# Kernel tuning notes

Measured on AMD Instinct MI355X. Metric: run time of the kernel, lower is better.

## Reference

```python
import jax, jax.numpy as jnp
import numpy as np
from math import pi
from jax.scipy.linalg import expm

N_QUBITS = 9
DIM = 256
BATCH = 64
HID = (4 + DIM) // 2
D = 2 ** N_QUBITS
INTERACTION_WEIGHT = 866.0 / (3.0 ** 6)


def setup_inputs() -> dict:
    key = jax.random.key(0)
    k = jax.random.split(key, 6)
    x = jax.random.normal(k[0], (BATCH, DIM), dtype=jnp.float32)
    mask_batch = jax.random.uniform(k[1], (BATCH, N_QUBITS), dtype=jnp.float32)
    upper = (jax.random.uniform(k[2], (N_QUBITS, N_QUBITS)) < 0.4).astype(jnp.float32)
    upper = jnp.triu(upper, 1)
    adj = upper + upper.T  # symmetric 0/1, zero diagonal
    W1 = jax.random.normal(k[3], (DIM, HID), dtype=jnp.float32) / np.sqrt(DIM).astype(np.float32)
    b1 = jnp.zeros((HID,), jnp.float32)
    W2 = jax.random.normal(k[4], (HID, 4), dtype=jnp.float32) / np.sqrt(HID).astype(np.float32)
    b2 = jnp.zeros((4,), jnp.float32)
    return {"x": x, "mask_batch": mask_batch, "adj": adj, "W1": W1, "b1": b1, "W2": W2, "b2": b2}


def _forward(x, mask_batch, adj, W1, b1, W2, b2):
    c64 = jnp.complex64
    n = N_QUBITS
    b = x.shape[0]
    # varyer MLP -> [raw_omega, delta, raw_phi, raw_time]
    v = jax.nn.relu(x @ W1 + b1) @ W2 + b2
    omega = jax.nn.softplus(v[:, 0])
    delta = v[:, 1]
    phi = jnp.mod(v[:, 2], 2.0 * pi)
    t = jax.nn.softplus(v[:, 3])
    sx = jnp.array([[0, 1], [1, 0]], dtype=c64)
    sy = jnp.array([[0, -1j], [1j, 0]], dtype=c64)
    nop = jnp.array([[1, 0], [0, 0]], dtype=c64)  # (I + sigma_z)/2
    # single-qubit Hamiltonian, (b, 2, 2)
    h = ((omega / 2)[:, None, None].astype(c64)
         * (jnp.cos(phi)[:, None, None] * sx - jnp.sin(phi)[:, None, None] * sy)
         - delta[:, None, None].astype(c64) * nop)
    # H_single = sum_j mask[b,j] * (I_{2^j} (x) h[b] (x) I_{2^{n-1-j}})
    H = jnp.zeros((b, D, D), dtype=c64)
    for j in range(n):  # structural loop over qubits (n fixed, small)
        L, R = 2 ** j, 2 ** (n - 1 - j)
        Ej = jnp.einsum('pq,bxy,rs->bpxrqys',
                        jnp.eye(L, dtype=c64), h, jnp.eye(R, dtype=c64)).reshape(b, D, D)
        H = H + mask_batch[:, j, None, None].astype(c64) * Ej
    # Interaction term: n_i n_j operators are diagonal in the computational basis.
    # kron ordering puts qubit 0 most significant; n_op = diag(1, 0) -> occ = 1 - bit.
    s = jnp.arange(D)
    bit = (s[:, None] >> (n - 1 - jnp.arange(n))[None, :]) & 1  # (D, n)
    occ = (1 - bit).astype(jnp.float32)
    Wmat = INTERACTION_WEIGHT * adj[None] * mask_batch[:, :, None] * mask_batch[:, None, :]  # (b,n,n)
    diag = jnp.einsum('bij,si,sj->bs', Wmat, occ, occ)  # (b, D)
    idx = jnp.arange(D)
    H = H.at[:, idx, idx].add(diag.astype(c64))
    # time evolution: psi = expm(-i t H) |0...0>  (first column of the propagator)
    M = (-1j) * t[:, None, None].astype(c64) * H
    exp_h = jax.vmap(expm)(M)
    return exp_h[:, :, 0]


def reference(x, mask_batch, adj, W1, b1, W2, b2):
    return _forward(x, mask_batch, adj, W1, b1, W2, b2)
```

## Files before the change

### kernel.cpp

```cpp
#include <hip/hip_runtime.h>
#include <math.h>

#define NQ     9
#define NDIM   256
#define NHID   130
#define NST    512
#define NBATCH 64
#define MCAP   460

__device__ __forceinline__ float softplusf(float x) {
    return (x > 0.f) ? (x + log1pf(expf(-x))) : log1pf(expf(x));
}

template<int CTRL>
__device__ __forceinline__ float dpp_f(float v) {
    int i = __float_as_int(v);
    return __int_as_float(__builtin_amdgcn_update_dpp(i, i, CTRL, 0xF, 0xF, false));
}
__device__ __forceinline__ float swzx16(float v) {
    return __int_as_float(__builtin_amdgcn_ds_swizzle(__float_as_int(v), 0x401F));
}
__device__ __forceinline__ float bperm(int addr, float v) {
    return __int_as_float(__builtin_amdgcn_ds_bpermute(addr, __float_as_int(v)));
}

typedef unsigned uint2v __attribute__((ext_vector_type(2)));

__device__ __forceinline__ float lx16(float v, bool hi) {
#if __has_builtin(__builtin_amdgcn_permlane16_swap)
    uint2v r = __builtin_amdgcn_permlane16_swap(__float_as_uint(v), __float_as_uint(v), false, false);
    return __uint_as_float(hi ? r[0] : r[1]);
#else
    return swzx16(v);
#endif
}
__device__ __forceinline__ float lx32(float v, bool hi, int bpaddr) {
#if __has_builtin(__builtin_amdgcn_permlane32_swap)
    uint2v r = __builtin_amdgcn_permlane32_swap(__float_as_uint(v), __float_as_uint(v), false, false);
    return __uint_as_float(hi ? r[0] : r[1]);
#else
    return bperm(bpaddr, v);
#endif
}

#define MV(NR, CR)                                                            \
  do {                                                                        \
    _Pragma("unroll")                                                         \
    for (int r = 0; r < 8; ++r) {                                             \
      const float a = CR[r];                                                  \
      float yr = dg2[r] * a;                                                  \
      yr = fmaf(in2[0], CR[r^1], yr);                                         \
      yr = fmaf(in2[1], CR[r^2], yr);                                         \
      yr = fmaf(in2[2], CR[r^4], yr);                                         \
      yr = fmaf(cx2[0], dpp_f<0xB1>(a), yr);                                  \
      yr = fmaf(cx2[1], dpp_f<0x4E>(a), yr);                                  \
      const float a7 = dpp_f<0x141>(a);                                       \
      yr = fmaf(cx2[2], dpp_f<0x1B>(a7), yr);                                 \
      yr = fmaf(cx2[3], dpp_f<0x140>(a7), yr);                                \
      yr = fmaf(cx2[4], lx16(a, h16), yr);                                    \
      yr = fmaf(cx2[5], lx32(a, h32, bpaddr), yr);                            \
      NR[r] = yr - NR[r];                                                     \
    }                                                                         \
  } while (0)

#define COEF(P, K)                                                            \
  do { const float ck = 2.0f * jlf[K];                                        \
    switch ((K) & 3) {                                                        \
      case 0: _Pragma("unroll") for (int r=0;r<8;++r) accr[r] += ck*P[r]; break; \
      case 1: _Pragma("unroll") for (int r=0;r<8;++r) acci[r] -= ck*P[r]; break; \
      case 2: _Pragma("unroll") for (int r=0;r<8;++r) accr[r] -= ck*P[r]; break; \
      case 3: _Pragma("unroll") for (int r=0;r<8;++r) acci[r] += ck*P[r]; break; \
    }                                                                         \
  } while (0)

__global__ __launch_bounds__(256) void fused_kernel(
    const float* __restrict__ x,    const float* __restrict__ mask,
    const float* __restrict__ adj,  const float* __restrict__ W1,
    const float* __restrict__ b1,   const float* __restrict__ W2,
    const float* __restrict__ b2,   float* __restrict__ out)
{
    const int b    = blockIdx.x;
    const int tid  = threadIdx.x;
    const int w    = tid >> 6;
    const int lane = tid & 63;

    __shared__ __align__(16) float w1s[NDIM * NHID];
    __shared__ float xs[NDIM];
    __shared__ float hs[NHID + 2];
    __shared__ float vs[4];
    __shared__ float ms[NQ];
    __shared__ float Wm[81];
    __shared__ double Ssh;

    float Dsum[8], mo[8];

    if (w != 0) {
        const int t0 = tid - 64;
        const float4* W14 = (const float4*)W1;
        float4* d4 = (float4*)w1s;
        for (int i = t0; i < (NDIM*NHID)/4; i += 192) d4[i] = W14[i];
        if (t0 < NDIM/4) ((float4*)xs)[t0] = ((const float4*)(x + b*NDIM))[t0];
    } else {
        if (lane < NQ) ms[lane] = mask[b*NQ + lane];
        for (int e = lane; e < 81; e += 64) {
            int i = e / 9, j = e % 9;
            Wm[e] = (866.0f/729.0f) * adj[e] * ms[i] * ms[j];
        }
        #pragma unroll
        for (int r = 0; r < 8; ++r) {
            const int s = (lane << 3) | r;
            float d = 0.f, m = 0.f;
            #pragma unroll
            for (int i = 0; i < NQ; ++i) {
                float oi = ((s >> (8 - i)) & 1) ? 0.f : 1.f;
                m = fmaf(ms[i], oi, m);
                float row = 0.f;
                #pragma unroll
                for (int j = 0; j < NQ; ++j) {
                    float oj = ((s >> (8 - j)) & 1) ? 0.f : 1.f;
                    row = fmaf(Wm[i*9 + j], oj, row);
                }
                d = fmaf(oi, row, d);
            }
            Dsum[r] = d; mo[r] = m;
        }
    }
    __syncthreads();

    if (tid < NHID) {
        float a0 = b1[tid], a1 = 0.f;
        #pragma unroll 8
        for (int i = 0; i < NDIM; i += 2) {
            a0 = fmaf(xs[i],     w1s[i*NHID + tid],       a0);
            a1 = fmaf(xs[i + 1], w1s[(i + 1)*NHID + tid], a1);
        }
        hs[tid] = fmaxf(a0 + a1, 0.f);
    }
    __syncthreads();

    {
        float p = hs[lane]      * W2[lane*4 + w]
                + hs[lane + 64] * W2[(lane + 64)*4 + w];
        if (lane < 2) p += hs[128 + lane] * W2[(128 + lane)*4 + w];
        #pragma unroll
        for (int off = 32; off; off >>= 1) p += __shfl_down(p, off);
        if (lane == 0) vs[w] = p + b2[w];
    }
    __syncthreads();

    if (w != 0) return;

    double* fd  = (double*)w1s;
    float*  jlf = w1s + 2*(MCAP + 8);

    const float omega = softplusf(vs[0]);
    const float delta = vs[1];
    const float phi   = vs[2];
    const float t     = softplusf(vs[3]);
    const float halfw = 0.5f * omega;

    float Dd[8];
    #pragma unroll
    for (int r = 0; r < 8; ++r) Dd[r] = Dsum[r] - delta * mo[r];

    float mx = Dd[0], mn = Dd[0];
    #pragma unroll
    for (int r = 1; r < 8; ++r) { mx = fmaxf(mx, Dd[r]); mn = fminf(mn, Dd[r]); }
    #pragma unroll
    for (int off = 1; off < 64; off <<= 1) {
        mx = fmaxf(mx, __shfl_xor(mx, off));
        mn = fminf(mn, __shfl_xor(mn, off));
    }
    float sm = 0.f;
    #pragma unroll
    for (int j = 0; j < NQ; ++j) sm += ms[j];
    const float c0   = 0.5f * (mx + mn);
    const float rho  = (0.5f * (mx - mn) + halfw * sm) * 1.003f;
    const float rhoE = fmaxf(rho, 1e-20f);
    const float zc   = t * rho;

    int M;
    const bool tiny = (zc < 0.5f);
    if (tiny) M = 8;
    else {
        M = (int)ceilf(zc + 3.5f * cbrtf(zc + 4.f) + 4.f);
        if (M > MCAP) M = MCAP;
    }

    if (tiny) {
        if (lane <= 8) {
            const float zh = 0.5f * zc;
            const float q  = zh * zh;
            float fact = 1.f;
            for (int i = 2; i <= lane; ++i) fact *= (float)i;
            const float pw = (lane == 0) ? 1.f : powf(zh, (float)lane);
            jlf[lane] = (pw / fact) *
                (1.f - q/(float)(lane+1) + 0.5f*q*q/(float)((lane+1)*(lane+2)));
        }
    } else {
        if (lane == 0) {
            const double zz  = (double)zc;
            const double inv = 1.0 / zz;
            const int   M2   = M + 20 + M/10;
            double fkp1 = 0.0, fk = 1e-30;
            for (int k = M2; k >= 1; --k) {
                double fkm1 = 2.0 * (double)k * inv * fk - fkp1;
                fkp1 = fk; fk = fkm1;
                const int idx = k - 1;
                if (idx <= M) fd[idx] = fk;
            }
            double S = fd[0];
            for (int idx = 2; idx <= M; idx += 2) S += 2.0 * fd[idx];
            Ssh = S;
        }
        for (int k = lane; k <= M; k += 64) jlf[k] = (float)(fd[k] / Ssh);
    }

    const float two_rho = 2.0f / rhoE;
    float dg2[8];
    #pragma unroll
    for (int r = 0; r < 8; ++r) dg2[r] = (Dd[r] - c0) * two_rho;
    float cx2[6];
    #pragma unroll
    for (int q = 0; q < 6; ++q) cx2[q] = ms[5 - q] * halfw * two_rho;
    float in2[3];
    #pragma unroll
    for (int p = 0; p < 3; ++p) in2[p] = ms[8 - p] * halfw * two_rho;
    const int  bpaddr = (lane ^ 32) << 2;
    const bool h16    = (lane & 16) != 0;
    const bool h32    = (lane & 32) != 0;

    float p0[8], p1[8], accr[8], acci[8];
    #pragma unroll
    for (int r = 0; r < 8; ++r) { p0[r] = 0.f; p1[r] = 0.f; acci[r] = 0.f; }
    p0[0] = (lane == 0) ? 1.f : 0.f;

    const float J0 = jlf[0];
    #pragma unroll
    for (int r = 0; r < 8; ++r) accr[r] = J0 * p0[r];

    MV(p1, p0);
    #pragma unroll
    for (int r = 0; r < 8; ++r) p1[r] *= 0.5f;
    { const float c1 = 2.0f * jlf[1];
      #pragma unroll
      for (int r = 0; r < 8; ++r) acci[r] -= c1 * p1[r]; }

    int k = 2;
    while (k <= M) {
        MV(p0, p1);
        COEF(p0, k);
        ++k;
        if (k > M) break;
        MV(p1, p0);
        COEF(p1, k);
        ++k;
    }

    const float base = t * c0;
    const float pcl  = (float)__popc(lane);
    float o[8];
    #pragma unroll
    for (int r = 0; r < 8; ++r) {
        const float beta = base + phi * (pcl + (float)__popc(r));
        float sb, cbta;
        __sincosf(beta, &sb, &cbta);
        o[r] = accr[r]*cbta + acci[r]*sb;
    }
    float4* o4 = (float4*)(out + b*NST + (lane << 3));
    o4[0] = make_float4(o[0], o[1], o[2], o[3]);
    o4[1] = make_float4(o[4], o[5], o[6], o[7]);
}

extern "C" void kernel_launch(void* const* d_in, const int* in_sizes, int n_in,
                              void* d_out, int out_size, void* d_ws, size_t ws_size,
                              hipStream_t stream) {
    const float *x = nullptr, *msk = nullptr, *adj = nullptr,
                *W1 = nullptr, *b1 = nullptr, *W2 = nullptr, *b2 = nullptr;
    for (int i = 0; i < n_in; ++i) {
        const float* p = (const float*)d_in[i];
        switch (in_sizes[i]) {
            case 16384: x   = p; break;
            case 576:   msk = p; break;
            case 81:    adj = p; break;
            case 33280: W1  = p; break;
            case 130:   b1  = p; break;
            case 520:   W2  = p; break;
            case 4:     b2  = p; break;
            default: break;
        }
    }
    fused_kernel<<<NBATCH, 256, 0, stream>>>(x, msk, adj, W1, b1, W2, b2,
                                             (float*)d_out);
}
```

Before: 28.15 us.

## Factor interaction diagonal per lane and spread W1 staging across all waves

Wave 0 no longer computes the interaction diagonal while the other waves load W1. All 256 threads now stage W1, x, mask and adj together, and wave 0 computes the diagonal after the MLP. The diagonal is factored by splitting each lane's 6 high bits from the 3 low bits of the row index, so the shared 6-bit part is computed once per lane and the 8 rows only add cheap cross terms. This cuts redundant quadratic-form work and gives the copy loop more threads, but the diagonal work moves onto the serial tail after the MLP instead of overlapping with the load.

```diff
diff --git a/kernel.cpp b/kernel.cpp
--- a/kernel.cpp
+++ b/kernel.cpp
@@ -89,41 +89,18 @@
     __shared__ float hs[NHID + 2];
     __shared__ float vs[4];
     __shared__ float ms[NQ];
+    __shared__ float adjs[81];
     __shared__ float Wm[81];
     __shared__ double Ssh;
 
-    float Dsum[8], mo[8];
-
-    if (w != 0) {
-        const int t0 = tid - 64;
+    {
         const float4* W14 = (const float4*)W1;
         float4* d4 = (float4*)w1s;
-        for (int i = t0; i < (NDIM*NHID)/4; i += 192) d4[i] = W14[i];
-        if (t0 < NDIM/4) ((float4*)xs)[t0] = ((const float4*)(x + b*NDIM))[t0];
-    } else {
-        if (lane < NQ) ms[lane] = mask[b*NQ + lane];
-        for (int e = lane; e < 81; e += 64) {
-            int i = e / 9, j = e % 9;
-            Wm[e] = (866.0f/729.0f) * adj[e] * ms[i] * ms[j];
-        }
-        #pragma unroll
-        for (int r = 0; r < 8; ++r) {
-            const int s = (lane << 3) | r;
-            float d = 0.f, m = 0.f;
-            #pragma unroll
-            for (int i = 0; i < NQ; ++i) {
-                float oi = ((s >> (8 - i)) & 1) ? 0.f : 1.f;
-                m = fmaf(ms[i], oi, m);
-                float row = 0.f;
-                #pragma unroll
-                for (int j = 0; j < NQ; ++j) {
-                    float oj = ((s >> (8 - j)) & 1) ? 0.f : 1.f;
-                    row = fmaf(Wm[i*9 + j], oj, row);
-                }
-                d = fmaf(oi, row, d);
-            }
-            Dsum[r] = d; mo[r] = m;
-        }
+        #pragma unroll 4
+        for (int i = tid; i < (NDIM*NHID)/4; i += 256) d4[i] = W14[i];
+        if (tid < NDIM/4) ((float4*)xs)[tid] = ((const float4*)(x + b*NDIM))[tid];
+        if (tid >= 64 && tid < 64 + NQ) ms[tid - 64] = mask[b*NQ + (tid - 64)];
+        if (tid >= 128 && tid < 128 + 81) adjs[tid - 128] = adj[tid - 128];
     }
     __syncthreads();
 
@@ -153,15 +130,45 @@
     double* fd  = (double*)w1s;
     float*  jlf = w1s + 2*(MCAP + 8);
 
+    for (int e = lane; e < 81; e += 64) {
+        int i = e / 9, j = e % 9;
+        Wm[e] = (866.0f/729.0f) * adjs[e] * ms[i] * ms[j];
+    }
+
     const float omega = softplusf(vs[0]);
     const float delta = vs[1];
     const float phi   = vs[2];
     const float t     = softplusf(vs[3]);
     const float halfw = 0.5f * omega;
 
+    float oL[6];
+    #pragma unroll
+    for (int i = 0; i < 6; ++i) oL[i] = ((lane >> (5 - i)) & 1) ? 0.f : 1.f;
+    float t1 = 0.f, moL = 0.f;
+    for (int i = 0; i < 6; ++i) {
+        moL = fmaf(ms[i], oL[i], moL);
+        float row = 0.f;
+        for (int j = 0; j < 6; ++j) row = fmaf(Wm[i*9 + j], oL[j], row);
+        t1 = fmaf(oL[i], row, t1);
+    }
+    float g[3];
+    for (int p = 0; p < 3; ++p) {
+        float gp = 0.f;
+        for (int i = 0; i < 6; ++i) gp = fmaf(Wm[i*9 + 6 + p], oL[i], gp);
+        g[p] = gp;
+    }
+    const float w67 = Wm[6*9 + 7], w68 = Wm[6*9 + 8], w78 = Wm[7*9 + 8];
     float Dd[8];
     #pragma unroll
-    for (int r = 0; r < 8; ++r) Dd[r] = Dsum[r] - delta * mo[r];
+    for (int r = 0; r < 8; ++r) {
+        const float o0 = (r & 4) ? 0.f : 1.f;
+        const float o1 = (r & 2) ? 0.f : 1.f;
+        const float o2 = (r & 1) ? 0.f : 1.f;
+        const float cross = g[0]*o0 + g[1]*o1 + g[2]*o2;
+        const float rr    = w67*o0*o1 + w68*o0*o2 + w78*o1*o2;
+        const float mo_r  = moL + ms[6]*o0 + ms[7]*o1 + ms[8]*o2;
+        Dd[r] = t1 + 2.f*(cross + rr) - delta*mo_r;
+    }
 
     float mx = Dd[0], mn = Dd[0];
     #pragma unroll
@@ -172,7 +179,6 @@
         mn = fminf(mn, __shfl_xor(mn, off));
     }
     float sm = 0.f;
-    #pragma unroll
     for (int j = 0; j < NQ; ++j) sm += ms[j];
     const float c0   = 0.5f * (mx + mn);
     const float rho  = (0.5f * (mx - mn) + halfw * sm) * 1.003f;
```

Measured after the change: 25.30 us. -10.1%, faster.
